# Performance work log

Measured on AMD Instinct MI355X. Metric: run time of the kernel, lower is better.

Reference implementation:

```python
import jax, jax.numpy as jnp
import numpy as np

B, L, A = 256, 512, 40          # proteins, residues per protein, atoms per drug
FD, FT, LD = 78, 54, 128        # drug feat, protein feat, latent dim
P = L + 1                       # residues + 1 appended drug super-node


def setup_inputs() -> dict:
    key = jax.random.key(0)
    ks = iter(jax.random.split(key, 48))
    Nd = B * A
    # drug graphs: chain bonds, both directions
    i = np.arange(A - 1)
    s = np.concatenate([i, i + 1]); d = np.concatenate([i + 1, i])
    off = (np.arange(B) * A)[:, None]
    drug_ei = jnp.asarray(np.stack([(s[None] + off).ravel(), (d[None] + off).ravel()]), jnp.int32)
    drug_batch = jnp.asarray(np.repeat(np.arange(B), A), jnp.int32)
    # protein graphs: residue chain + drug super-node (local idx L) connected to all residues in order
    r = np.arange(L - 1)
    ps = np.concatenate([r, r + 1, np.full(L, L), np.arange(L)])
    pd = np.concatenate([r + 1, r, np.arange(L), np.full(L, L)])
    poff = (np.arange(B) * P)[:, None]
    prot_ei = jnp.asarray(np.stack([(ps[None] + poff).ravel(), (pd[None] + poff).ravel()]), jnp.int32)
    prot_batch = jnp.asarray(np.repeat(np.arange(B), P), jnp.int32)
    E2 = B * (2 * (L - 1) + 2 * L)

    def lin(fi, fo):
        return jax.random.normal(next(ks), (fi, fo), jnp.float32) / np.float32(np.sqrt(fi))

    def vec(fo):
        return jnp.zeros((fo,), jnp.float32)

    return dict(
        drug_x=jax.random.normal(next(ks), (Nd, FD), jnp.float32),
        drug_ei=drug_ei, drug_batch=drug_batch,
        prot_x=jax.random.normal(next(ks), (B * P, FT), jnp.float32),
        prot_ei=prot_ei, prot_batch=prot_batch,
        prot_ea=jax.random.uniform(next(ks), (E2,), jnp.float32),
        W_c1d=lin(FD, FD), b_c1d=vec(FD),
        W_c2d=lin(FD, 2 * FD), b_c2d=vec(2 * FD),
        W_rd_g=lin(2 * FD, 2 * FD), b_rd_g=vec(2 * FD), W_rd_l=lin(2 * FD, 2 * FD),
        W_fg1d=lin(2 * FD, 1024), b_fg1d=vec(1024),
        W_fg2d=lin(1024, FT), b_fg2d=vec(FT),
        W_fg3d=lin(FT, 2 * LD), b_fg3d=vec(2 * LD),
        W_att1=lin(FT, FT), b_att1=vec(FT),
        W_att2=lin(FT, 1), b_att2=vec(1),
        W_c1t=lin(FT, LD), b_c1t=vec(LD),
        W_c2t=lin(LD, 2 * LD), b_c2t=vec(2 * LD),
        W_rt_g=lin(2 * LD, 2 * LD), b_rt_g=vec(2 * LD), W_rt_l=lin(2 * LD, 2 * LD),
        W_fg1t=lin(2 * LD, 1024), b_fg1t=vec(1024),
        W_fg2t=lin(1024, 2 * LD), b_fg2t=vec(2 * LD),
        W_fc1=lin(4 * LD, 1024), b_fc1=vec(1024),
        W_fc2=lin(1024, 512), b_fc2=vec(512),
        W_out=lin(512, 1), b_out=vec(1),
    )


def _gcn(x, W, b, src, dst, ew, n):
    # PyG GCNConv: symmetric norm with self-loops (fill value 1), optional edge weights
    h = x @ W
    deg = jax.ops.segment_sum(ew, dst, num_segments=n) + 1.0
    dinv = jax.lax.rsqrt(deg)
    norm = dinv[src] * ew * dinv[dst]
    agg = jax.ops.segment_sum(h[src] * norm[:, None], dst, num_segments=n)
    return agg + h * (dinv * dinv)[:, None] + b


def _rblock(x, Wg, bg, Wl, src, dst, ew, n):
    h = jax.nn.relu(_gcn(x, Wg, bg, src, dst, ew, n))
    return jax.nn.relu(h @ Wl + x)


def reference(drug_x, drug_ei, drug_batch, prot_x, prot_ei, prot_batch, prot_ea,
              W_c1d, b_c1d, W_c2d, b_c2d, W_rd_g, b_rd_g, W_rd_l,
              W_fg1d, b_fg1d, W_fg2d, b_fg2d, W_fg3d, b_fg3d,
              W_att1, b_att1, W_att2, b_att2,
              W_c1t, b_c1t, W_c2t, b_c2t, W_rt_g, b_rt_g, W_rt_l,
              W_fg1t, b_fg1t, W_fg2t, b_fg2t,
              W_fc1, b_fc1, W_fc2, b_fc2, W_out, b_out):
    relu = jax.nn.relu
    Nd, N2 = drug_x.shape[0], prot_x.shape[0]
    sd, dd = drug_ei[0], drug_ei[1]
    ewd = jnp.ones(sd.shape[0], drug_x.dtype)
    x = relu(_gcn(drug_x, W_c1d, b_c1d, sd, dd, ewd, Nd))
    x = relu(_gcn(x, W_c2d, b_c2d, sd, dd, ewd, Nd))
    for _ in range(4):  # shared-weight residual block applied num_rblock times
        x = _rblock(x, W_rd_g, b_rd_g, W_rd_l, sd, dd, ewd, Nd)
    xg = jax.ops.segment_max(x, drug_batch, num_segments=B)  # global max pool
    x = relu(xg @ W_fg1d + b_fg1d)
    x = x @ W_fg2d + b_fg2d                                   # [B, FT]
    x_chg = relu(x @ W_fg3d + b_fg3d)                          # [B, 2*LD]
    # vectorized per-protein attention (replaces the python loop over prot_lens)
    res = prot_x.reshape(B, P, FT)[:, :L]                      # residues only
    att = jnp.tanh(res @ W_att1 + b_att1) @ W_att2 + b_att2    # [B, L, 1]
    att = jax.nn.softmax(att[..., 0], axis=1)                  # [B, L]
    att_node = jnp.concatenate([att, jnp.zeros((B, 1), att.dtype)], 1).reshape(-1)
    drug_idx = (jnp.arange(B) + 1) * P - 1
    is_drug = jnp.zeros((N2,), bool).at[drug_idx].set(True)
    st, dt = prot_ei[0], prot_ei[1]
    # edges touching a drug super-node get that residue's attention weight
    ea = jnp.where(is_drug[st], att_node[dt], jnp.where(is_drug[dt], att_node[st], prot_ea))
    x2 = prot_x.at[drug_idx].set(x)                            # inject drug embeddings
    x2 = relu(_gcn(x2, W_c1t, b_c1t, st, dt, ea, N2))
    x2 = relu(_gcn(x2, W_c2t, b_c2t, st, dt, ea, N2))
    ew1 = jnp.ones(st.shape[0], x2.dtype)
    for _ in range(4):
        x2 = _rblock(x2, W_rt_g, b_rt_g, W_rt_l, st, dt, ew1, N2)
    x2r = x2.reshape(B, P, 2 * LD)
    x2g = x2r[:, :L].max(axis=1)                               # gmp over residues (drug node masked out)
    drug_after = x2r[:, L]
    x2v = relu(x2g @ W_fg1t + b_fg1t) @ W_fg2t + b_fg2t
    xm = jnp.maximum(drug_after, x_chg)                        # max_pool1d(kernel=2) over the pair
    xc = jnp.concatenate([xm, x2v], 1)
    xc = relu(xc @ W_fc1 + b_fc1)
    xc = relu(xc @ W_fc2 + b_fc2)
    return xc @ W_out + b_out
```

## Files before the change

### kernel.cpp

```cpp
#include <hip/hip_runtime.h>
#include <cstdio>

#define B_   256
#define L_   512
#define A_   40
#define FD_  78
#define FT_  54
#define LD_  128
#define P_   513
#define ND_  (B_*A_)
#define N2_  (B_*P_)
#define EB_  2046

typedef __attribute__((ext_vector_type(8))) short short8;
typedef __attribute__((ext_vector_type(4))) float floatx4;
typedef unsigned short u16;

__device__ __forceinline__ short f2bf(float f) {
    union { float f; unsigned u; } v; v.f = f;
    unsigned u = v.u;
    u += 0x7fff + ((u >> 16) & 1);
    return (short)(u >> 16);
}
__device__ __forceinline__ float bf2f(u16 s) {
    union { unsigned u; float f; } v; v.u = ((unsigned)s) << 16; return v.f;
}

#define TBK 32
#define LDK 40
#define UBS 264

__global__ __launch_bounds__(256) void gemm_mfma_k(
    const float* __restrict__ A, const short* __restrict__ WT,
    float* __restrict__ C, int M, int N, int K, int Kp)
{
    __shared__ short As[128 * LDK];
    __shared__ short Bs[128 * LDK];
    const int bm = blockIdx.y * 128;
    const int bn = blockIdx.x * 128;
    const int tid  = threadIdx.x;
    const int wave = tid >> 6, lane = tid & 63;
    const int wm = (wave >> 1) * 64, wn = (wave & 1) * 64;
    const int lrow = lane & 15, quad = lane >> 4;

    floatx4 acc[4][4] = {};

    for (int k0 = 0; k0 < Kp; k0 += TBK) {
#pragma unroll
        for (int it = 0; it < 2; ++it) {
            int g   = it * 256 + tid;
            int row = g >> 2, kg = g & 3;
            int kb  = k0 + kg * 8;
            const float* arow = A + (size_t)(bm + row) * K + kb;
            short8 av;
#pragma unroll
            for (int j = 0; j < 8; ++j) av[j] = (kb + j < K) ? f2bf(arow[j]) : (short)0;
            *(short8*)&As[row * LDK + kg * 8] = av;
            *(short8*)&Bs[row * LDK + kg * 8] = *(const short8*)(WT + (size_t)(bn + row) * Kp + kb);
        }
        __syncthreads();
        short8 af[4], bfv[4];
#pragma unroll
        for (int i = 0; i < 4; ++i)
            af[i] = *(short8*)&As[(wm + i * 16 + lrow) * LDK + quad * 8];
#pragma unroll
        for (int j = 0; j < 4; ++j)
            bfv[j] = *(short8*)&Bs[(wn + j * 16 + lrow) * LDK + quad * 8];
#pragma unroll
        for (int i = 0; i < 4; ++i)
#pragma unroll
            for (int j = 0; j < 4; ++j)
                acc[i][j] = __builtin_amdgcn_mfma_f32_16x16x32_bf16(af[i], bfv[j], acc[i][j], 0, 0, 0);
        __syncthreads();
    }
#pragma unroll
    for (int i = 0; i < 4; ++i) {
        int grow0 = bm + wm + i * 16 + quad * 4;
#pragma unroll
        for (int j = 0; j < 4; ++j) {
            int col = bn + wn + j * 16 + lrow;
            size_t base = (size_t)grow0 * N + col;
#pragma unroll
            for (int r = 0; r < 4; ++r)
                C[base + (size_t)r * N] = acc[i][j][r];
        }
    }
}

__global__ __launch_bounds__(256) void gemm_bb_k(
    const u16* __restrict__ A, int lda, const short* __restrict__ WT, int Kp,
    const u16* __restrict__ resid, u16* __restrict__ C, int N, int act)
{
    __shared__ short As[128 * LDK];
    __shared__ short Bs[128 * LDK];
    const int bm = blockIdx.y * 128;
    const int bn = blockIdx.x * 128;
    const int tid  = threadIdx.x;
    const int wave = tid >> 6, lane = tid & 63;
    const int wm = (wave >> 1) * 64, wn = (wave & 1) * 64;
    const int lrow = lane & 15, quad = lane >> 4;

    floatx4 acc[4][4] = {};

    for (int k0 = 0; k0 < Kp; k0 += TBK) {
#pragma unroll
        for (int it = 0; it < 2; ++it) {
            int g   = it * 256 + tid;
            int row = g >> 2, kg = g & 3;
            int kb  = k0 + kg * 8;
            *(short8*)&As[row * LDK + kg * 8] = *(const short8*)(A + (size_t)(bm + row) * lda + kb);
            *(short8*)&Bs[row * LDK + kg * 8] = *(const short8*)(WT + (size_t)(bn + row) * Kp + kb);
        }
        __syncthreads();
        short8 af[4], bfv[4];
#pragma unroll
        for (int i = 0; i < 4; ++i)
            af[i] = *(short8*)&As[(wm + i * 16 + lrow) * LDK + quad * 8];
#pragma unroll
        for (int j = 0; j < 4; ++j)
            bfv[j] = *(short8*)&Bs[(wn + j * 16 + lrow) * LDK + quad * 8];
#pragma unroll
        for (int i = 0; i < 4; ++i)
#pragma unroll
            for (int j = 0; j < 4; ++j)
                acc[i][j] = __builtin_amdgcn_mfma_f32_16x16x32_bf16(af[i], bfv[j], acc[i][j], 0, 0, 0);
        __syncthreads();
    }
#pragma unroll
    for (int i = 0; i < 4; ++i) {
        int grow0 = bm + wm + i * 16 + quad * 4;
#pragma unroll
        for (int j = 0; j < 4; ++j) {
            int col = bn + wn + j * 16 + lrow;
            size_t base = (size_t)grow0 * N + col;
#pragma unroll
            for (int r = 0; r < 4; ++r) {
                float v = acc[i][j][r];
                size_t idx = base + (size_t)r * N;
                if (resid) v += bf2f(resid[idx]);
                if (act)   v = fmaxf(v, 0.f);
                C[idx] = (u16)f2bf(v);
            }
        }
    }
}

template<int KT>
__global__ __launch_bounds__(256, 3) void gemm_n256pw_k(
    const u16* __restrict__ A, const short* __restrict__ WT,
    const u16* __restrict__ resid, u16* __restrict__ C, int act,
    const float* __restrict__ cInF, float* __restrict__ Wacc)
{
    constexpr int K = KT * TBK;
    __shared__ short As[64 * LDK];
    __shared__ short Bs[256 * LDK];
    const int bm = blockIdx.x * 64;
    const int tid  = threadIdx.x;
    const int wave = tid >> 6, lane = tid & 63;
    const int wn = wave * 64;
    const int lrow = lane & 15, quad = lane >> 4;
    const int srow = tid >> 2, skg = tid & 3;

    floatx4 acc[4][4] = {};

    short8 aR[KT];
#pragma unroll
    for (int kt = 0; kt < KT; ++kt)
        aR[kt] = *(const short8*)(A + (size_t)(bm + srow) * K + kt * TBK + skg * 8);
    short8 bReg[4];
#pragma unroll
    for (int it = 0; it < 4; ++it)
        bReg[it] = *(const short8*)(WT + (size_t)(it * 64 + srow) * K + skg * 8);

#pragma unroll
    for (int kt = 0; kt < KT; ++kt) {
        *(short8*)&As[srow * LDK + skg * 8] = aR[kt];
#pragma unroll
        for (int it = 0; it < 4; ++it)
            *(short8*)&Bs[(it * 64 + srow) * LDK + skg * 8] = bReg[it];
        __syncthreads();
        if (kt + 1 < KT) {
            int kn = (kt + 1) * TBK;
#pragma unroll
            for (int it = 0; it < 4; ++it)
                bReg[it] = *(const short8*)(WT + (size_t)(it * 64 + srow) * K + kn + skg * 8);
        }
        short8 af[4], bfv[4];
#pragma unroll
        for (int i = 0; i < 4; ++i)
            af[i] = *(short8*)&As[(i * 16 + lrow) * LDK + quad * 8];
#pragma unroll
        for (int j = 0; j < 4; ++j)
            bfv[j] = *(short8*)&Bs[(wn + j * 16 + lrow) * LDK + quad * 8];
#pragma unroll
        for (int i = 0; i < 4; ++i)
#pragma unroll
            for (int j = 0; j < 4; ++j)
                acc[i][j] = __builtin_amdgcn_mfma_f32_16x16x32_bf16(af[i], bfv[j], acc[i][j], 0, 0, 0);
        __syncthreads();
    }
#pragma unroll
    for (int i = 0; i < 4; ++i) {
        int grow0 = bm + i * 16 + quad * 4;
#pragma unroll
        for (int j = 0; j < 4; ++j) {
            int col = wn + j * 16 + lrow;
            size_t base = (size_t)grow0 * 256 + col;
#pragma unroll
            for (int r = 0; r < 4; ++r) {
                float v = acc[i][j][r];
                size_t idx = base + (size_t)r * 256;
                if (resid) v += bf2f(resid[idx]);
                if (act)   v = fmaxf(v, 0.f);
                C[idx] = (u16)f2bf(v);
            }
        }
    }
    if (cInF) {
        const int b0 = bm / P_;
        const int b1 = (bm + 63) / P_;
        float s0[4] = {0.f, 0.f, 0.f, 0.f};
        float s1[4] = {0.f, 0.f, 0.f, 0.f};
#pragma unroll
        for (int i = 0; i < 4; ++i) {
#pragma unroll
            for (int r = 0; r < 4; ++r) {
                int grow = bm + i * 16 + quad * 4 + r;
                float ci = cInF[grow];
                bool hi = (grow / P_) != b0;
#pragma unroll
                for (int j = 0; j < 4; ++j) {
                    float v = ci * acc[i][j][r];
                    if (hi) s1[j] += v; else s0[j] += v;
                }
            }
        }
#pragma unroll
        for (int j = 0; j < 4; ++j) {
            s0[j] += __shfl_xor(s0[j], 16);
            s0[j] += __shfl_xor(s0[j], 32);
            s1[j] += __shfl_xor(s1[j], 16);
            s1[j] += __shfl_xor(s1[j], 32);
        }
        if (quad == 0) {
#pragma unroll
            for (int j = 0; j < 4; ++j) {
                int col = wn + j * 16 + lrow;
                atomicAdd(&Wacc[(size_t)b0 * 256 + col], s0[j]);
                if (b1 != b0) atomicAdd(&Wacc[(size_t)b1 * 256 + col], s1[j]);
            }
        }
    }
}

static inline void gemm_n256(const u16* A, int K, const short* WT,
                             const u16* resid, u16* C, int act,
                             const float* cInF, float* Wacc, hipStream_t s)
{
    dim3 g(N2_ / 64), b(256);
    if (K == 128)
        hipLaunchKernelGGL((gemm_n256pw_k<4>), g, b, 0, s, A, WT, resid, C, act, cInF, Wacc);
    else
        hipLaunchKernelGGL((gemm_n256pw_k<8>), g, b, 0, s, A, WT, resid, C, act, cInF, Wacc);
}

template<int KT>
__global__ __launch_bounds__(256, 2) void fused_res_k(
    const u16* __restrict__ X, const short* __restrict__ WTg,
    const short* __restrict__ WTl, const u16* __restrict__ Udrug,
    const float* __restrict__ cPc, const float* __restrict__ cNc,
    const float* __restrict__ cDc, const float* __restrict__ cSc,
    const float* __restrict__ cInF, const float* __restrict__ bias_g,
    float* __restrict__ Wacc, u16* __restrict__ Xn)
{
    constexpr int K = KT * TBK;
    __shared__ short Ub[80 * UBS];
    __shared__ short As[80 * LDK];
    const int bm    = blockIdx.x * 64;
    const int gbase = bm - 8;
    const int tid   = threadIdx.x;
    const int wave  = tid >> 6, lane = tid & 63;
    const int wn    = wave * 64;
    const int lrow  = lane & 15, quad = lane >> 4;
    const int srow  = tid >> 2, skg = tid & 3;

    int g1 = gbase + srow;
    g1 = g1 < 0 ? 0 : g1;
    const u16* ap1 = X + (size_t)g1 * K + skg * 8;
    int g2 = gbase + 64 + srow;
    g2 = g2 >= N2_ ? N2_ - 1 : g2;
    const u16* ap2 = X + (size_t)g2 * K + skg * 8;
    const bool w0 = (wave == 0);

    const short* bgp0 = WTg + (size_t)(wn +  0 + lrow) * K + quad * 8;
    const short* bgp1 = WTg + (size_t)(wn + 16 + lrow) * K + quad * 8;
    const short* bgp2 = WTg + (size_t)(wn + 32 + lrow) * K + quad * 8;
    const short* bgp3 = WTg + (size_t)(wn + 48 + lrow) * K + quad * 8;

    floatx4 acc[5][4] = {};
    short8 aP1[2], aP2[2], bP[2][4];
    aP1[0] = *(const short8*)ap1;
    if (w0) aP2[0] = *(const short8*)ap2;
    bP[0][0] = *(const short8*)bgp0;
    bP[0][1] = *(const short8*)bgp1;
    bP[0][2] = *(const short8*)bgp2;
    bP[0][3] = *(const short8*)bgp3;

#pragma unroll
    for (int kt = 0; kt < KT; ++kt) {
        const int cur = kt & 1, nxt = cur ^ 1;
        *(short8*)&As[srow * LDK + skg * 8] = aP1[cur];
        if (w0) *(short8*)&As[(64 + srow) * LDK + skg * 8] = aP2[cur];
        __syncthreads();
        if (kt + 1 < KT) {
            const int kn = (kt + 1) * TBK;
            aP1[nxt] = *(const short8*)(ap1 + kn);
            if (w0) aP2[nxt] = *(const short8*)(ap2 + kn);
            bP[nxt][0] = *(const short8*)(bgp0 + kn);
            bP[nxt][1] = *(const short8*)(bgp1 + kn);
            bP[nxt][2] = *(const short8*)(bgp2 + kn);
            bP[nxt][3] = *(const short8*)(bgp3 + kn);
        }
        short8 af[5];
#pragma unroll
        for (int i = 0; i < 5; ++i)
            af[i] = *(short8*)&As[(i * 16 + lrow) * LDK + quad * 8];
#pragma unroll
        for (int i = 0; i < 5; ++i)
#pragma unroll
            for (int j = 0; j < 4; ++j)
                acc[i][j] = __builtin_amdgcn_mfma_f32_16x16x32_bf16(af[i], bP[cur][j], acc[i][j], 0, 0, 0);
        __syncthreads();
    }

    {
        const int b0 = bm / P_;
        const int b1 = (bm + 63) / P_;
        float s0[4] = {0.f, 0.f, 0.f, 0.f};
        float s1[4] = {0.f, 0.f, 0.f, 0.f};
#pragma unroll
        for (int i = 0; i < 5; ++i) {
#pragma unroll
            for (int r = 0; r < 4; ++r) {
                int wr = i * 16 + quad * 4 + r;
                if (wr >= 8 && wr < 72) {
                    int grow = gbase + wr;
                    float ci = cInF[grow];
                    bool hi = (grow / P_) != b0;
#pragma unroll
                    for (int j = 0; j < 4; ++j) {
                        float v = ci * acc[i][j][r];
                        if (hi) s1[j] += v; else s0[j] += v;
                    }
                }
            }
        }
#pragma unroll
        for (int j = 0; j < 4; ++j) {
            s0[j] += __shfl_xor(s0[j], 16);
            s0[j] += __shfl_xor(s0[j], 32);
            s1[j] += __shfl_xor(s1[j], 16);
            s1[j] += __shfl_xor(s1[j], 32);
        }
        if (quad == 0) {
#pragma unroll
            for (int j = 0; j < 4; ++j) {
                int col = wn + j * 16 + lrow;
                atomicAdd(&Wacc[(size_t)b0 * 256 + col], s0[j]);
                if (b1 != b0) atomicAdd(&Wacc[(size_t)b1 * 256 + col], s1[j]);
            }
        }
    }

#pragma unroll
    for (int i = 0; i < 5; ++i)
#pragma unroll
        for (int r = 0; r < 4; ++r) {
            int wr = i * 16 + quad * 4 + r;
#pragma unroll
            for (int j = 0; j < 4; ++j)
                Ub[wr * UBS + wn + j * 16 + lrow] = f2bf(acc[i][j][r]);
        }
    __syncthreads();

    const int r    = bm + srow;
    const int bl   = r / P_;
    const int irow = r - bl * P_;
    const bool isD = (irow == L_);
    const float cs = isD ? 0.f : cSc[r];
    const float cp = isD ? 0.f : cPc[r];
    const float cn = isD ? 0.f : cNc[r];
    const float cd = isD ? 0.f : cDc[r];
    const u16* udp = Udrug + (size_t)bl * 256;

    const short* blp0 = WTl + (size_t)(wn +  0 + lrow) * K + quad * 8;
    const short* blp1 = WTl + (size_t)(wn + 16 + lrow) * K + quad * 8;
    const short* blp2 = WTl + (size_t)(wn + 32 + lrow) * K + quad * 8;
    const short* blp3 = WTl + (size_t)(wn + 48 + lrow) * K + quad * 8;

    floatx4 acc2[4][4] = {};
    short8 bl2[2][4];
    bl2[0][0] = *(const short8*)blp0;
    bl2[0][1] = *(const short8*)blp1;
    bl2[0][2] = *(const short8*)blp2;
    bl2[0][3] = *(const short8*)blp3;

#pragma unroll
    for (int kt = 0; kt < KT; ++kt) {
        const int cur = kt & 1, nxt = cur ^ 1;
        const int c0 = kt * TBK + skg * 8;
        short8 uS = *(short8*)&Ub[(8 + srow) * UBS + c0];
        short8 uM = *(short8*)&Ub[(7 + srow) * UBS + c0];
        short8 uP = *(short8*)&Ub[(9 + srow) * UBS + c0];
        short8 ud = *(const short8*)(udp + c0);
        float4 bi0 = *(const float4*)(bias_g + c0);
        float4 bi1 = *(const float4*)(bias_g + c0 + 4);
        float bv[8] = {bi0.x, bi0.y, bi0.z, bi0.w, bi1.x, bi1.y, bi1.z, bi1.w};
        short8 av;
#pragma unroll
        for (int e = 0; e < 8; ++e) {
            float v = cs * bf2f((u16)uS[e]) + cp * bf2f((u16)uM[e])
                    + cn * bf2f((u16)uP[e]) + cd * bf2f((u16)ud[e]) + bv[e];
            av[e] = f2bf(fmaxf(v, 0.f));
        }
        *(short8*)&As[srow * LDK + skg * 8] = av;
        __syncthreads();
        if (kt + 1 < KT) {
            const int kn = (kt + 1) * TBK;
            bl2[nxt][0] = *(const short8*)(blp0 + kn);
            bl2[nxt][1] = *(const short8*)(blp1 + kn);
            bl2[nxt][2] = *(const short8*)(blp2 + kn);
            bl2[nxt][3] = *(const short8*)(blp3 + kn);
        }
        short8 af2[4];
#pragma unroll
        for (int i = 0; i < 4; ++i)
            af2[i] = *(short8*)&As[(i * 16 + lrow) * LDK + quad * 8];
#pragma unroll
        for (int i = 0; i < 4; ++i)
#pragma unroll
            for (int j = 0; j < 4; ++j)
                acc2[i][j] = __builtin_amdgcn_mfma_f32_16x16x32_bf16(af2[i], bl2[cur][j], acc2[i][j], 0, 0, 0);
        __syncthreads();
    }

#pragma unroll
    for (int i = 0; i < 4; ++i) {
        int grow0 = bm + i * 16 + quad * 4;
#pragma unroll
        for (int j = 0; j < 4; ++j) {
            int col = wn + j * 16 + lrow;
            size_t base = (size_t)grow0 * 256 + col;
#pragma unroll
            for (int r2 = 0; r2 < 4; ++r2) {
                float v = acc2[i][j][r2];
                size_t idx = base + (size_t)r2 * 256;
                v += bf2f(X[idx]);
                v = fmaxf(v, 0.f);
                Xn[idx] = (u16)f2bf(v);
            }
        }
    }
}

__global__ __launch_bounds__(256) void udrug_k(
    const u16* __restrict__ Xold, const short* __restrict__ WTg,
    u16* __restrict__ Udrug)
{
    __shared__ float xr[256];
    int b = blockIdx.x, t = threadIdx.x;
    size_t rD = (size_t)b * P_ + L_;
    xr[t] = bf2f(Xold[rD * 256 + t]);
    __syncthreads();
    const short* wrow = WTg + (size_t)t * 256;
    float v = 0.f;
    for (int k = 0; k < 256; k += 8) {
        short8 w = *(const short8*)(wrow + k);
#pragma unroll
        for (int e = 0; e < 8; ++e) v += xr[k + e] * bf2f((u16)w[e]);
    }
    Udrug[(size_t)b * 256 + t] = (u16)f2bf(v);
}

__global__ __launch_bounds__(256) void drug_row_k(
    const float* __restrict__ Wacc, const u16* __restrict__ Udrug,
    const float* __restrict__ cSc, const float* __restrict__ bias_g,
    const short* __restrict__ WTl, const u16* __restrict__ Xold,
    u16* __restrict__ Xn)
{
    __shared__ float a2[256];
    int b = blockIdx.x, t = threadIdx.x;
    size_t rD = (size_t)b * P_ + L_;
    float u = bf2f(Udrug[(size_t)b * 256 + t]);
    float av = fmaxf(Wacc[(size_t)b * 256 + t] + cSc[rD] * u + bias_g[t], 0.f);
    a2[t] = bf2f((u16)f2bf(av));
    __syncthreads();
    const short* wrow = WTl + (size_t)t * 256;
    float v = 0.f;
    for (int k = 0; k < 256; k += 8) {
        short8 w = *(const short8*)(wrow + k);
#pragma unroll
        for (int e = 0; e < 8; ++e) v += a2[k + e] * bf2f((u16)w[e]);
    }
    v += bf2f(Xold[rD * 256 + t]);
    Xn[rD * 256 + t] = (u16)f2bf(fmaxf(v, 0.f));
}

__global__ void wt_cvt_k(const float* __restrict__ W, short* __restrict__ WT,
                         int K, int Nreal, int Kp, int Ntot)
{
    int idx = blockIdx.x * 256 + threadIdx.x;
    if (idx >= Ntot * Kp) return;
    int n = idx / Kp, k = idx - n * Kp;
    WT[idx] = (k < K && n < Nreal) ? f2bf(W[(size_t)k * Nreal + n]) : (short)0;
}

#define BM 64
#define BN 64
#define BKK 16
__global__ __launch_bounds__(256) void gemm_k(
    const float* __restrict__ Amat, const float* __restrict__ Wmat,
    const float* __restrict__ bias, const float* __restrict__ resid,
    float* __restrict__ Cmat, int M, int N, int K, int act)
{
    __shared__ float As[BKK][BM + 4];
    __shared__ float Ws[BKK][BN];
    const int bm = blockIdx.y * BM;
    const int bn = blockIdx.x * BN;
    const int tx = threadIdx.x, ty = threadIdx.y;
    const int tid = ty * 16 + tx;
    float acc[4][4] = {};

    for (int k0 = 0; k0 < K; k0 += BKK) {
#pragma unroll
        for (int j = 0; j < 4; ++j) {
            int l = tid + 256 * j;
            int m = l >> 4, kk = l & 15;
            int gm = bm + m, gk = k0 + kk;
            As[kk][m] = (gm < M && gk < K) ? Amat[(size_t)gm * K + gk] : 0.f;
        }
#pragma unroll
        for (int j = 0; j < 4; ++j) {
            int l = tid + 256 * j;
            int kk = l >> 6, n = l & 63;
            int gk = k0 + kk, gn = bn + n;
            Ws[kk][n] = (gk < K && gn < N) ? Wmat[(size_t)gk * N + gn] : 0.f;
        }
        __syncthreads();
#pragma unroll
        for (int k = 0; k < BKK; ++k) {
            float4 a4 = *(const float4*)&As[k][ty * 4];
            float4 w4 = *(const float4*)&Ws[k][tx * 4];
            float av[4] = {a4.x, a4.y, a4.z, a4.w};
            float wv[4] = {w4.x, w4.y, w4.z, w4.w};
#pragma unroll
            for (int i = 0; i < 4; ++i)
#pragma unroll
                for (int j = 0; j < 4; ++j)
                    acc[i][j] = fmaf(av[i], wv[j], acc[i][j]);
        }
        __syncthreads();
    }
#pragma unroll
    for (int i = 0; i < 4; ++i) {
        int gm = bm + ty * 4 + i;
        if (gm >= M) continue;
#pragma unroll
        for (int j = 0; j < 4; ++j) {
            int gn = bn + tx * 4 + j;
            if (gn >= N) continue;
            float v = acc[i][j];
            if (bias)  v += bias[gn];
            if (resid) v += resid[(size_t)gm * N + gn];
            if (act)   v = fmaxf(v, 0.f);
            Cmat[(size_t)gm * N + gn] = v;
        }
    }
}

static inline void gemm(const float* A, const float* W, const float* bias,
                        const float* resid, float* C, int M, int N, int K, int act,
                        hipStream_t s)
{
    dim3 g((N + BN - 1) / BN, (M + BM - 1) / BM), b(16, 16);
    hipLaunchKernelGGL(gemm_k, g, b, 0, s, A, W, bias, resid, C, M, N, K, act);
}

__global__ __launch_bounds__(256) void gemm_skA_k(
    const float* __restrict__ Amat, const float* __restrict__ Wmat,
    float* __restrict__ part, int M, int N, int K, int Kc)
{
    __shared__ float As[BKK][BM + 4];
    __shared__ float Ws[BKK][BN];
    const int bm = blockIdx.y * BM;
    const int bn = blockIdx.x * BN;
    const int sk = blockIdx.z;
    const int kb0  = sk * Kc;
    const int kend = min(K, kb0 + Kc);
    const int tx = threadIdx.x, ty = threadIdx.y;
    const int tid = ty * 16 + tx;
    float acc[4][4] = {};

    for (int k0 = kb0; k0 < kend; k0 += BKK) {
#pragma unroll
        for (int j = 0; j < 4; ++j) {
            int l = tid + 256 * j;
            int m = l >> 4, kk = l & 15;
            int gm = bm + m, gk = k0 + kk;
            As[kk][m] = (gm < M && gk < kend) ? Amat[(size_t)gm * K + gk] : 0.f;
        }
#pragma unroll
        for (int j = 0; j < 4; ++j) {
            int l = tid + 256 * j;
            int kk = l >> 6, n = l & 63;
            int gk = k0 + kk, gn = bn + n;
            Ws[kk][n] = (gk < kend && gn < N) ? Wmat[(size_t)gk * N + gn] : 0.f;
        }
        __syncthreads();
#pragma unroll
        for (int k = 0; k < BKK; ++k) {
            float4 a4 = *(const float4*)&As[k][ty * 4];
            float4 w4 = *(const float4*)&Ws[k][tx * 4];
            float av[4] = {a4.x, a4.y, a4.z, a4.w};
            float wv[4] = {w4.x, w4.y, w4.z, w4.w};
#pragma unroll
            for (int i = 0; i < 4; ++i)
#pragma unroll
                for (int j = 0; j < 4; ++j)
                    acc[i][j] = fmaf(av[i], wv[j], acc[i][j]);
        }
        __syncthreads();
    }
#pragma unroll
    for (int i = 0; i < 4; ++i) {
        int gm = bm + ty * 4 + i;
        if (gm >= M) continue;
#pragma unroll
        for (int j = 0; j < 4; ++j) {
            int gn = bn + tx * 4 + j;
            if (gn >= N) continue;
            part[((size_t)sk * M + gm) * N + gn] = acc[i][j];
        }
    }
}

__global__ void gemm_skB_k(const float* __restrict__ part, const float* __restrict__ bias,
                           float* __restrict__ C, int M, int N, int SK, int act)
{
    int idx = blockIdx.x * 256 + threadIdx.x;
    if (idx >= M * N) return;
    int n = idx % N;
    float v = bias ? bias[n] : 0.f;
    for (int s = 0; s < SK; ++s) v += part[(size_t)s * M * N + idx];
    if (act) v = fmaxf(v, 0.f);
    C[idx] = v;
}

static inline void gemm_sk(const float* A, const float* W, const float* bias,
                           float* C, float* skbuf, int M, int N, int K, int SK, int act,
                           hipStream_t s)
{
    int Kc = (K + SK - 1) / SK;
    dim3 g((N + 63) / 64, (M + 63) / 64, SK), b(16, 16);
    hipLaunchKernelGGL(gemm_skA_k, g, b, 0, s, A, W, skbuf, M, N, K, Kc);
    hipLaunchKernelGGL(gemm_skB_k, dim3((M * N + 255) / 256), dim3(256), 0, s,
                       skbuf, bias, C, M, N, SK, act);
}

__global__ void drug_agg_k(const float* __restrict__ h, const float* __restrict__ bias,
                           float* __restrict__ out, int F)
{
    int r = blockIdx.x;
    int a = r % A_;
    int t = threadIdx.x;
    if (t >= F) return;
    const float DI2 = 0.70710678118654752f;
    const float DI3 = 0.57735026918962576f;
    float da = (a == 0 || a == A_ - 1) ? DI2 : DI3;
    const float* hs = h + (size_t)r * F;
    float v = da * da * hs[t] + bias[t];
    if (a > 0) {
        float dp = (a - 1 == 0) ? DI2 : DI3;
        v += dp * da * hs[t - F];
    }
    if (a < A_ - 1) {
        float dn = (a + 1 == A_ - 1) ? DI2 : DI3;
        v += dn * da * hs[t + F];
    }
    out[(size_t)r * F + t] = fmaxf(v, 0.f);
}

__global__ void drug_max_k(const float* __restrict__ x, float* __restrict__ xg)
{
    int b = blockIdx.x, t = threadIdx.x;
    if (t >= 2 * FD_) return;
    const float* xb = x + (size_t)b * A_ * (2 * FD_);
    float m = -INFINITY;
    for (int a = 0; a < A_; ++a) m = fmaxf(m, xb[a * (2 * FD_) + t]);
    xg[b * (2 * FD_) + t] = m;
}

__global__ __launch_bounds__(256) void att_dot_k(
    const float* __restrict__ Hs, const float* __restrict__ b1,
    const float* __restrict__ W2, const float* __restrict__ b2,
    float* __restrict__ scores)
{
    int w = threadIdx.x >> 6, lane = threadIdx.x & 63;
    float b1v = (lane < FT_) ? b1[lane] : 0.f;
    float w2v = (lane < FT_) ? W2[lane] : 0.f;
    float b2v = b2[0];
    int base = blockIdx.x * 64 + w * 16;
    for (int rr = 0; rr < 16; ++rr) {
        int r = base + rr;
        float v = 0.f;
        if (lane < FT_) v = tanhf(Hs[(size_t)r * 128 + lane] + b1v) * w2v;
#pragma unroll
        for (int o = 32; o; o >>= 1) v += __shfl_down(v, o);
        if (lane == 0) {
            int bl = r / P_, i = r - bl * P_;
            if (i < L_) scores[bl * L_ + i] = v + b2v;
        }
    }
}

__global__ __launch_bounds__(512) void softmax_k(
    const float* __restrict__ scores, float* __restrict__ att, float* __restrict__ attsum)
{
    int b = blockIdx.x, t = threadIdx.x;
    __shared__ float sm[8];
    __shared__ float bcast;
    float v = scores[b * L_ + t];
    float m = v;
#pragma unroll
    for (int o = 32; o; o >>= 1) m = fmaxf(m, __shfl_down(m, o));
    if ((t & 63) == 0) sm[t >> 6] = m;
    __syncthreads();
    if (t == 0) { float mm = sm[0]; for (int i = 1; i < 8; ++i) mm = fmaxf(mm, sm[i]); bcast = mm; }
    __syncthreads();
    float mx = bcast;
    float e = expf(v - mx);
    float s = e;
#pragma unroll
    for (int o = 32; o; o >>= 1) s += __shfl_down(s, o);
    __syncthreads();
    if ((t & 63) == 0) sm[t >> 6] = s;
    __syncthreads();
    if (t == 0) { float ss = 0; for (int i = 0; i < 8; ++i) ss += sm[i]; bcast = ss; }
    __syncthreads();
    float a = e / bcast;
    att[b * L_ + t] = a;
    float s2 = a;
#pragma unroll
    for (int o = 32; o; o >>= 1) s2 += __shfl_down(s2, o);
    __syncthreads();
    if ((t & 63) == 0) sm[t >> 6] = s2;
    __syncthreads();
    if (t == 0) { float ss = 0; for (int i = 0; i < 8; ++i) ss += sm[i]; attsum[b] = ss; }
}

__global__ void coef_deg_k(const float* __restrict__ prot_ea, const float* __restrict__ att,
                           const float* __restrict__ attsum, float* __restrict__ dinv, int use_ea)
{
    int r = blockIdx.x * 256 + threadIdx.x;
    if (r >= N2_) return;
    int b = r / P_, i = r - b * P_;
    float deg;
    if (i == L_) {
        deg = 1.f + (use_ea ? attsum[b] : (float)L_);
    } else {
        float wP = (i >= 1)      ? (use_ea ? prot_ea[b * EB_ + (i - 1)]   : 1.f) : 0.f;
        float wN = (i <= L_ - 2) ? (use_ea ? prot_ea[b * EB_ + 511 + i]   : 1.f) : 0.f;
        float wD = use_ea ? att[b * L_ + i] : 1.f;
        deg = 1.f + wP + wN + wD;
    }
    dinv[r] = rsqrtf(deg);
}

__global__ void coef_k(const float* __restrict__ dinv, const float* __restrict__ prot_ea,
                       const float* __restrict__ att, float* __restrict__ cP, float* __restrict__ cN,
                       float* __restrict__ cD, float* __restrict__ cS, float* __restrict__ cIn,
                       float* __restrict__ cInF, int use_ea)
{
    int r = blockIdx.x * 256 + threadIdx.x;
    if (r >= N2_) return;
    int b = r / P_, i = r - b * P_;
    float di = dinv[r];
    cS[r] = di * di;
    if (i == L_) { cP[r] = 0.f; cN[r] = 0.f; cD[r] = 0.f; cInF[r] = 0.f; return; }
    float wP = (i >= 1)      ? (use_ea ? prot_ea[b * EB_ + (i - 1)] : 1.f) : 0.f;
    float wN = (i <= L_ - 2) ? (use_ea ? prot_ea[b * EB_ + 511 + i] : 1.f) : 0.f;
    float wD = use_ea ? att[b * L_ + i] : 1.f;
    float dD = dinv[b * P_ + L_];
    cP[r] = (i >= 1)      ? dinv[r - 1] * wP * di : 0.f;
    cN[r] = (i <= L_ - 2) ? dinv[r + 1] * wN * di : 0.f;
    cD[r] = dD * wD * di;
    float ci = di * wD * dD;
    cIn[b * L_ + i] = ci;
    cInF[r] = ci;
}

template<int F>
__global__ __launch_bounds__(256) void prot_agg_res_k(
    const u16* __restrict__ h, const float* __restrict__ cP,
    const float* __restrict__ cN, const float* __restrict__ cD,
    const float* __restrict__ cS, const float* __restrict__ cIn,
    const float* __restrict__ bias, u16* __restrict__ outp,
    float* __restrict__ Wacc)
{
    constexpr int G = F / 8;
    constexpr int RPB = 256 / G;
    __shared__ float pacc[RPB * F];
    int t = threadIdx.x;
    int rl = t / G, g = t - rl * G;
    int base = blockIdx.x * RPB;
    int r = base + rl;
    int bl = r / P_, i = r - bl * P_;
    int f0 = g * 8;
    const u16* hs = h + (size_t)r * F + f0;
    if (i == L_) {
#pragma unroll
        for (int e = 0; e < 8; ++e) pacc[rl * F + f0 + e] = 0.f;
    } else {
        const u16* hd = h + ((size_t)bl * P_ + L_) * F + f0;
        float cs = cS[r], cd = cD[r], cp = cP[r], cn = cN[r];
        float ci = cIn[bl * L_ + i];
        short8 vs = *(const short8*)hs;
        short8 vd = *(const short8*)hd;
        short8 vp = *(const short8*)(hs - (i > 0 ? F : 0));
        short8 vn = *(const short8*)(hs + F);
        short8 ov;
#pragma unroll
        for (int e = 0; e < 8; ++e) {
            float hv = bf2f((u16)vs[e]);
            pacc[rl * F + f0 + e] = ci * hv;
            float v = cs * hv + cd * bf2f((u16)vd[e]) + bias[f0 + e];
            v += cp * bf2f((u16)vp[e]);
            v += cn * bf2f((u16)vn[e]);
            ov[e] = f2bf(fmaxf(v, 0.f));
        }
        *(short8*)(outp + (size_t)r * F + f0) = ov;
    }
    __syncthreads();
    int f = t;
    if (f < F) {
        int b0   = base / P_;
        int bend = (base + RPB - 1) / P_;
        float s0 = 0.f, s1 = 0.f;
#pragma unroll
        for (int rr = 0; rr < RPB; ++rr) {
            float v = pacc[rr * F + f];
            if ((base + rr) / P_ == b0) s0 += v; else s1 += v;
        }
        atomicAdd(&Wacc[(size_t)b0 * F + f], s0);
        if (bend != b0) atomicAdd(&Wacc[(size_t)bend * F + f], s1);
    }
}

__global__ void drug_fin_k(const float* __restrict__ Wacc, const u16* __restrict__ h,
                           const float* __restrict__ cS, const float* __restrict__ bias,
                           u16* __restrict__ outp, int F)
{
    int bl = blockIdx.x, t = threadIdx.x;
    if (t >= F) return;
    size_t rD = (size_t)bl * P_ + L_;
    float v = Wacc[(size_t)bl * F + t] + cS[rD] * bf2f(h[rD * F + t]) + bias[t];
    outp[rD * F + t] = (u16)f2bf(fmaxf(v, 0.f));
}

__global__ void xin_k(const float* __restrict__ prot_x, const float* __restrict__ t2d,
                      u16* __restrict__ Xin)
{
    int idx = blockIdx.x * 256 + threadIdx.x;
    if (idx >= N2_ * 64) return;
    int r = idx >> 6, t = idx & 63;
    int bl = r / P_, i = r - bl * P_;
    float v = 0.f;
    if (t < FT_) v = (i == L_) ? t2d[bl * FT_ + t] : prot_x[(size_t)r * FT_ + t];
    Xin[idx] = (u16)f2bf(v);
}

__global__ __launch_bounds__(256) void x2g_bf2_k(const u16* __restrict__ X,
                                                 float* __restrict__ x2g, float* __restrict__ da)
{
    __shared__ float red[2048];
    int t = threadIdx.x;
    int rl = t >> 5, g = t & 31;
    int bl = blockIdx.x, f0 = g * 8;
    const u16* xb = X + (size_t)bl * P_ * 256;
    float m[8];
#pragma unroll
    for (int e = 0; e < 8; ++e) m[e] = -INFINITY;
    for (int j = rl; j < L_; j += 8) {
        short8 v = *(const short8*)(xb + (size_t)j * 256 + f0);
#pragma unroll
        for (int e = 0; e < 8; ++e) m[e] = fmaxf(m[e], bf2f((u16)v[e]));
    }
#pragma unroll
    for (int e = 0; e < 8; ++e) red[rl * 256 + f0 + e] = m[e];
    __syncthreads();
    if (rl == 0) {
        short8 vd = *(const short8*)(xb + (size_t)L_ * 256 + f0);
#pragma unroll
        for (int e = 0; e < 8; ++e) {
            float v = red[f0 + e];
            for (int rr = 1; rr < 8; ++rr) v = fmaxf(v, red[rr * 256 + f0 + e]);
            x2g[bl * 256 + f0 + e] = v;
            da[bl * 256 + f0 + e] = bf2f((u16)vd[e]);
        }
    }
}

__global__ void build_xc_k(const float* __restrict__ da, const float* __restrict__ x_chg,
                           const float* __restrict__ x2v, float* __restrict__ xc)
{
    int idx = blockIdx.x * 256 + threadIdx.x;
    if (idx >= B_ * 512) return;
    int b = idx >> 9, c = idx & 511;
    float v = (c < 256) ? fmaxf(da[b * 256 + c], x_chg[b * 256 + c])
                        : x2v[b * 256 + (c - 256)];
    xc[idx] = v;
}

__global__ __launch_bounds__(64) void out_k(const float* __restrict__ f2,
                                            const float* __restrict__ W,
                                            const float* __restrict__ bias,
                                            float* __restrict__ out)
{
    int row = blockIdx.x, t = threadIdx.x;
    float v = 0.f;
    for (int k = t; k < 512; k += 64) v = fmaf(f2[(size_t)row * 512 + k], W[k], v);
#pragma unroll
    for (int o = 32; o; o >>= 1) v += __shfl_down(v, o);
    if (t == 0) out[row] = v + bias[0];
}

extern "C" void kernel_launch(void* const* d_in, const int* in_sizes, int n_in,
                              void* d_out, int out_size, void* d_ws, size_t ws_size,
                              hipStream_t stream)
{
    const float* drug_x  = (const float*)d_in[0];
    const float* prot_x  = (const float*)d_in[3];
    const float* prot_ea = (const float*)d_in[6];
    const float* W_c1d = (const float*)d_in[7];   const float* b_c1d = (const float*)d_in[8];
    const float* W_c2d = (const float*)d_in[9];   const float* b_c2d = (const float*)d_in[10];
    const float* W_rd_g = (const float*)d_in[11]; const float* b_rd_g = (const float*)d_in[12];
    const float* W_rd_l = (const float*)d_in[13];
    const float* W_fg1d = (const float*)d_in[14]; const float* b_fg1d = (const float*)d_in[15];
    const float* W_fg2d = (const float*)d_in[16]; const float* b_fg2d = (const float*)d_in[17];
    const float* W_fg3d = (const float*)d_in[18]; const float* b_fg3d = (const float*)d_in[19];
    const float* W_att1 = (const float*)d_in[20]; const float* b_att1 = (const float*)d_in[21];
    const float* W_att2 = (const float*)d_in[22]; const float* b_att2 = (const float*)d_in[23];
    const float* W_c1t = (const float*)d_in[24];  const float* b_c1t = (const float*)d_in[25];
    const float* W_c2t = (const float*)d_in[26];  const float* b_c2t = (const float*)d_in[27];
    const float* W_rt_g = (const float*)d_in[28]; const float* b_rt_g = (const float*)d_in[29];
    const float* W_rt_l = (const float*)d_in[30];
    const float* W_fg1t = (const float*)d_in[31]; const float* b_fg1t = (const float*)d_in[32];
    const float* W_fg2t = (const float*)d_in[33]; const float* b_fg2t = (const float*)d_in[34];
    const float* W_fc1 = (const float*)d_in[35];  const float* b_fc1 = (const float*)d_in[36];
    const float* W_fc2 = (const float*)d_in[37];  const float* b_fc2 = (const float*)d_in[38];
    const float* W_out = (const float*)d_in[39];  const float* b_out = (const float*)d_in[40];
    float* out = (float*)d_out;

    float* ws = (float*)d_ws;
    size_t off = 0;
    auto alloc = [&](size_t n) {
        n = (n + 3) & ~(size_t)3;
        float* p = ws + off; off += n; return p;
    };

    u16* U = (u16*)alloc((size_t)N2_ * 128);
    u16* V = (u16*)alloc((size_t)N2_ * 128);
    u16* X = (u16*)alloc((size_t)N2_ * 128);
    u16* Xin = (u16*)alloc((size_t)N2_ * 32);
    float* Hs = (float*)U;
    float* Wacc = alloc(B_ * 256);
    u16* Udrug = (u16*)alloc(B_ * 128);
    float* dA = alloc((size_t)ND_ * 156);
    float* dB = alloc((size_t)ND_ * 156);
    float* dC = alloc((size_t)ND_ * 156);
    float* xg    = alloc(B_ * 156);
    float* t1d   = alloc(B_ * 1024);
    float* t2d   = alloc(B_ * FT_);
    float* x_chg = alloc(B_ * 256);
    float* scores = alloc(B_ * 512);
    float* att    = alloc(B_ * 512);
    float* attsum = alloc(B_);
    float* dinvE = alloc(N2_);
    float* cPE = alloc(N2_); float* cNE = alloc(N2_); float* cDE = alloc(N2_); float* cSE = alloc(N2_);
    float* cInE = alloc(B_ * 512);
    float* cInFE = alloc(N2_);
    float* dinvO = alloc(N2_);
    float* cPO = alloc(N2_); float* cNO = alloc(N2_); float* cDO = alloc(N2_); float* cSO = alloc(N2_);
    float* cInO = alloc(B_ * 512);
    float* cInFO = alloc(N2_);
    float* x2g = alloc(B_ * 256);
    float* dafter = alloc(B_ * 256);
    float* t1t = alloc(B_ * 1024);
    float* x2v = alloc(B_ * 256);
    float* xc  = alloc(B_ * 512);
    float* f1  = alloc(B_ * 1024);
    float* f2  = alloc(B_ * 512);
    float* skbuf = alloc((size_t)2 * 1024 * 1024);
    short* WT_c1t = (short*)alloc(128 * 64 / 2);
    short* WT_c2t = (short*)alloc(256 * 128 / 2);
    short* WT_rtg = (short*)alloc(256 * 256 / 2);
    short* WT_rtl = (short*)alloc(256 * 256 / 2);
    short* WT_att = (short*)alloc(128 * 64 / 2);

    if (off * sizeof(float) > ws_size) {
        fprintf(stderr, "kernel_launch: workspace too small: need %zu, have %zu\n",
                off * sizeof(float), ws_size);
        return;
    }

    hipLaunchKernelGGL(wt_cvt_k, dim3((128 * 64 + 255) / 256), dim3(256), 0, stream,  W_c1t, WT_c1t, FT_, 128, 64, 128);
    hipLaunchKernelGGL(wt_cvt_k, dim3((256 * 128 + 255) / 256), dim3(256), 0, stream, W_c2t, WT_c2t, 128, 256, 128, 256);
    hipLaunchKernelGGL(wt_cvt_k, dim3((256 * 256 + 255) / 256), dim3(256), 0, stream, W_rt_g, WT_rtg, 256, 256, 256, 256);
    hipLaunchKernelGGL(wt_cvt_k, dim3((256 * 256 + 255) / 256), dim3(256), 0, stream, W_rt_l, WT_rtl, 256, 256, 256, 256);
    hipLaunchKernelGGL(wt_cvt_k, dim3((128 * 64 + 255) / 256), dim3(256), 0, stream,  W_att1, WT_att, FT_, FT_, 64, 128);

    gemm(drug_x, W_c1d, nullptr, nullptr, dB, ND_, FD_, FD_, 0, stream);
    hipLaunchKernelGGL(drug_agg_k, dim3(ND_), dim3(128), 0, stream, dB, b_c1d, dA, FD_);
    gemm(dA, W_c2d, nullptr, nullptr, dB, ND_, 2 * FD_, FD_, 0, stream);
    hipLaunchKernelGGL(drug_agg_k, dim3(ND_), dim3(192), 0, stream, dB, b_c2d, dA, 2 * FD_);
    for (int it = 0; it < 4; ++it) {
        gemm(dA, W_rd_g, nullptr, nullptr, dB, ND_, 2 * FD_, 2 * FD_, 0, stream);
        hipLaunchKernelGGL(drug_agg_k, dim3(ND_), dim3(192), 0, stream, dB, b_rd_g, dC, 2 * FD_);
        gemm(dC, W_rd_l, nullptr, dA, dB, ND_, 2 * FD_, 2 * FD_, 1, stream);
        float* tmp = dA; dA = dB; dB = tmp;
    }
    hipLaunchKernelGGL(drug_max_k, dim3(B_), dim3(192), 0, stream, dA, xg);
    gemm_sk(xg,  W_fg1d, b_fg1d, t1d,   skbuf, B_, 1024, 156, 4, 1, stream);
    gemm_sk(t1d, W_fg2d, b_fg2d, t2d,   skbuf, B_, FT_, 1024, 16, 0, stream);
    gemm_sk(t2d, W_fg3d, b_fg3d, x_chg, skbuf, B_, 2 * LD_, FT_, 2, 1, stream);

    {
        dim3 g(1, N2_ / 128), b(256);
        hipLaunchKernelGGL(gemm_mfma_k, g, b, 0, stream, prot_x, WT_att, Hs, N2_, 128, FT_, 64);
    }
    hipLaunchKernelGGL(att_dot_k, dim3(N2_ / 64), dim3(256), 0, stream, Hs, b_att1, W_att2, b_att2, scores);
    hipLaunchKernelGGL(softmax_k, dim3(B_), dim3(512), 0, stream, scores, att, attsum);

    hipLaunchKernelGGL(coef_deg_k, dim3((N2_ + 255) / 256), dim3(256), 0, stream, prot_ea, att, attsum, dinvE, 1);
    hipLaunchKernelGGL(coef_k, dim3((N2_ + 255) / 256), dim3(256), 0, stream, dinvE, prot_ea, att, cPE, cNE, cDE, cSE, cInE, cInFE, 1);
    hipLaunchKernelGGL(coef_deg_k, dim3((N2_ + 255) / 256), dim3(256), 0, stream, prot_ea, att, attsum, dinvO, 0);
    hipLaunchKernelGGL(coef_k, dim3((N2_ + 255) / 256), dim3(256), 0, stream, dinvO, prot_ea, att, cPO, cNO, cDO, cSO, cInO, cInFO, 0);

    hipLaunchKernelGGL(xin_k, dim3((N2_ * 64 + 255) / 256), dim3(256), 0, stream, prot_x, t2d, Xin);

    {
        dim3 g(1, N2_ / 128), b(256);
        hipLaunchKernelGGL(gemm_bb_k, g, b, 0, stream, Xin, 64, WT_c1t, 64,
                           (const u16*)nullptr, U, 128, 0);
    }
    hipMemsetAsync(Wacc, 0, B_ * 128 * sizeof(float), stream);
    hipLaunchKernelGGL((prot_agg_res_k<128>), dim3(N2_ / 16), dim3(256), 0, stream,
                       U, cPE, cNE, cDE, cSE, cInE, b_c1t, V, Wacc);
    hipLaunchKernelGGL(drug_fin_k, dim3(B_), dim3(128), 0, stream, Wacc, U, cSE, b_c1t, V, 128);
    gemm_n256(V, 128, WT_c2t, (const u16*)nullptr, U, 0, nullptr, nullptr, stream);
    hipMemsetAsync(Wacc, 0, B_ * 256 * sizeof(float), stream);
    hipLaunchKernelGGL((prot_agg_res_k<256>), dim3(N2_ / 8), dim3(256), 0, stream,
                       U, cPE, cNE, cDE, cSE, cInE, b_c2t, X, Wacc);
    hipLaunchKernelGGL(drug_fin_k, dim3(B_), dim3(256), 0, stream, Wacc, U, cSE, b_c2t, X, 256);

    u16* Xc = X;
    u16* Xo = U;
    for (int it = 0; it < 4; ++it) {
        hipMemsetAsync(Wacc, 0, B_ * 256 * sizeof(float), stream);
        hipLaunchKernelGGL(udrug_k, dim3(B_), dim3(256), 0, stream, Xc, WT_rtg, Udrug);
        hipLaunchKernelGGL((fused_res_k<8>), dim3(N2_ / 64), dim3(256), 0, stream,
                           Xc, WT_rtg, WT_rtl, Udrug,
                           cPO, cNO, cDO, cSO, cInFO, b_rt_g, Wacc, Xo);
        hipLaunchKernelGGL(drug_row_k, dim3(B_), dim3(256), 0, stream,
                           Wacc, Udrug, cSO, b_rt_g, WT_rtl, Xc, Xo);
        u16* t = Xc; Xc = Xo; Xo = t;
    }

    hipLaunchKernelGGL(x2g_bf2_k, dim3(B_), dim3(256), 0, stream, Xc, x2g, dafter);

    gemm_sk(x2g, W_fg1t, b_fg1t, t1t, skbuf, B_, 1024, 256, 8, 1, stream);
    gemm_sk(t1t, W_fg2t, b_fg2t, x2v, skbuf, B_, 256, 1024, 16, 0, stream);
    hipLaunchKernelGGL(build_xc_k, dim3(B_ * 512 / 256), dim3(256), 0, stream, dafter, x_chg, x2v, xc);
    gemm_sk(xc, W_fc1, b_fc1, f1, skbuf, B_, 1024, 512, 8, 1, stream);
    gemm_sk(f1, W_fc2, b_fc2, f2, skbuf, B_, 512, 1024, 16, 1, stream);
    hipLaunchKernelGGL(out_k, dim3(B_), dim3(64), 0, stream, f2, W_out, b_out, out);
}
```

Baseline: 1.348 ms.

## Preload A tiles into registers, XOR-swizzle Ub, fuse udrug and memset into drug_row

In fused_res_k, all K-slices of the A rows are now loaded into registers up front instead of double-buffered per step. The padded Ub staging buffer is replaced by an unpadded XOR-swizzled layout to cut LDS bank conflicts and shared memory use. drug_row_k now zeroes Wacc and computes the next iteration's Udrug itself, so the per-iteration memset and udrug_k launches are removed. This adds register pressure, which may reduce occupancy, and adds serial work to the small drug_row kernel.

```diff
diff --git a/kernel.cpp b/kernel.cpp
--- a/kernel.cpp
+++ b/kernel.cpp
@@ -28,7 +28,6 @@
 
 #define TBK 32
 #define LDK 40
-#define UBS 264
 
 __global__ __launch_bounds__(256) void gemm_mfma_k(
     const float* __restrict__ A, const short* __restrict__ WT,
@@ -273,8 +272,9 @@
     const float* __restrict__ cInF, const float* __restrict__ bias_g,
     float* __restrict__ Wacc, u16* __restrict__ Xn)
 {
-    constexpr int K = KT * TBK;
-    __shared__ short Ub[80 * UBS];
+    constexpr int K   = KT * TBK;
+    constexpr int UBW = 256;
+    __shared__ short Ub[80 * UBW];
     __shared__ short As[80 * LDK];
     const int bm    = blockIdx.x * 64;
     const int gbase = bm - 8;
@@ -292,15 +292,24 @@
     const u16* ap2 = X + (size_t)g2 * K + skg * 8;
     const bool w0 = (wave == 0);
 
+    short8 aR1[KT];
+#pragma unroll
+    for (int kt = 0; kt < KT; ++kt)
+        aR1[kt] = *(const short8*)(ap1 + kt * TBK);
+    short8 aR2[KT];
+    if (w0) {
+#pragma unroll
+        for (int kt = 0; kt < KT; ++kt)
+            aR2[kt] = *(const short8*)(ap2 + kt * TBK);
+    }
+
     const short* bgp0 = WTg + (size_t)(wn +  0 + lrow) * K + quad * 8;
     const short* bgp1 = WTg + (size_t)(wn + 16 + lrow) * K + quad * 8;
     const short* bgp2 = WTg + (size_t)(wn + 32 + lrow) * K + quad * 8;
     const short* bgp3 = WTg + (size_t)(wn + 48 + lrow) * K + quad * 8;
 
     floatx4 acc[5][4] = {};
-    short8 aP1[2], aP2[2], bP[2][4];
-    aP1[0] = *(const short8*)ap1;
-    if (w0) aP2[0] = *(const short8*)ap2;
+    short8 bP[2][4];
     bP[0][0] = *(const short8*)bgp0;
     bP[0][1] = *(const short8*)bgp1;
     bP[0][2] = *(const short8*)bgp2;
@@ -309,13 +318,11 @@
 #pragma unroll
     for (int kt = 0; kt < KT; ++kt) {
         const int cur = kt & 1, nxt = cur ^ 1;
-        *(short8*)&As[srow * LDK + skg * 8] = aP1[cur];
-        if (w0) *(short8*)&As[(64 + srow) * LDK + skg * 8] = aP2[cur];
+        *(short8*)&As[srow * LDK + skg * 8] = aR1[kt];
+        if (w0) *(short8*)&As[(64 + srow) * LDK + skg * 8] = aR2[kt];
         __syncthreads();
         if (kt + 1 < KT) {
             const int kn = (kt + 1) * TBK;
-            aP1[nxt] = *(const short8*)(ap1 + kn);
-            if (w0) aP2[nxt] = *(const short8*)(ap2 + kn);
             bP[nxt][0] = *(const short8*)(bgp0 + kn);
             bP[nxt][1] = *(const short8*)(bgp1 + kn);
             bP[nxt][2] = *(const short8*)(bgp2 + kn);
@@ -377,9 +384,10 @@
 #pragma unroll
         for (int r = 0; r < 4; ++r) {
             int wr = i * 16 + quad * 4 + r;
+            int x  = (wr & 7) << 3;
 #pragma unroll
             for (int j = 0; j < 4; ++j)
-                Ub[wr * UBS + wn + j * 16 + lrow] = f2bf(acc[i][j][r]);
+                Ub[wr * UBW + ((wn + j * 16 + lrow) ^ x)] = f2bf(acc[i][j][r]);
         }
     __syncthreads();
 
@@ -405,13 +413,16 @@
     bl2[0][2] = *(const short8*)blp2;
     bl2[0][3] = *(const short8*)blp3;
 
+    const int rM = 7 + srow, rS = 8 + srow, rP = 9 + srow;
+    const int xM = (rM & 7) << 3, xS = (rS & 7) << 3, xP = (rP & 7) << 3;
+
 #pragma unroll
     for (int kt = 0; kt < KT; ++kt) {
         const int cur = kt & 1, nxt = cur ^ 1;
         const int c0 = kt * TBK + skg * 8;
-        short8 uS = *(short8*)&Ub[(8 + srow) * UBS + c0];
-        short8 uM = *(short8*)&Ub[(7 + srow) * UBS + c0];
-        short8 uP = *(short8*)&Ub[(9 + srow) * UBS + c0];
+        short8 uS = *(short8*)&Ub[rS * UBW + (c0 ^ xS)];
+        short8 uM = *(short8*)&Ub[rM * UBW + (c0 ^ xM)];
+        short8 uP = *(short8*)&Ub[rP * UBW + (c0 ^ xP)];
         short8 ud = *(const short8*)(udp + c0);
         float4 bi0 = *(const float4*)(bias_g + c0);
         float4 bi1 = *(const float4*)(bias_g + c0 + 4);
@@ -483,27 +494,42 @@
 }
 
 __global__ __launch_bounds__(256) void drug_row_k(
-    const float* __restrict__ Wacc, const u16* __restrict__ Udrug,
+    float* __restrict__ Wacc, u16* __restrict__ Udrug,
     const float* __restrict__ cSc, const float* __restrict__ bias_g,
-    const short* __restrict__ WTl, const u16* __restrict__ Xold,
-    u16* __restrict__ Xn)
+    const short* __restrict__ WTl, const short* __restrict__ WTg,
+    const u16* __restrict__ Xold, u16* __restrict__ Xn, int last)
 {
     __shared__ float a2[256];
+    __shared__ float xn[256];
     int b = blockIdx.x, t = threadIdx.x;
     size_t rD = (size_t)b * P_ + L_;
     float u = bf2f(Udrug[(size_t)b * 256 + t]);
     float av = fmaxf(Wacc[(size_t)b * 256 + t] + cSc[rD] * u + bias_g[t], 0.f);
+    Wacc[(size_t)b * 256 + t] = 0.f;
     a2[t] = bf2f((u16)f2bf(av));
     __syncthreads();
-    const short* wrow = WTl + (size_t)t * 256;
+    const short* wl = WTl + (size_t)t * 256;
     float v = 0.f;
     for (int k = 0; k < 256; k += 8) {
-        short8 w = *(const short8*)(wrow + k);
+        short8 w = *(const short8*)(wl + k);
 #pragma unroll
         for (int e = 0; e < 8; ++e) v += a2[k + e] * bf2f((u16)w[e]);
     }
     v += bf2f(Xold[rD * 256 + t]);
-    Xn[rD * 256 + t] = (u16)f2bf(fmaxf(v, 0.f));
+    u16 xb = (u16)f2bf(fmaxf(v, 0.f));
+    Xn[rD * 256 + t] = xb;
+    if (!last) {
+        xn[t] = bf2f(xb);
+        __syncthreads();
+        const short* wg = WTg + (size_t)t * 256;
+        float v2 = 0.f;
+        for (int k = 0; k < 256; k += 8) {
+            short8 w = *(const short8*)(wg + k);
+#pragma unroll
+            for (int e = 0; e < 8; ++e) v2 += xn[k + e] * bf2f((u16)w[e]);
+        }
+        Udrug[(size_t)b * 256 + t] = (u16)f2bf(v2);
+    }
 }
 
 __global__ void wt_cvt_k(const float* __restrict__ W, short* __restrict__ WT,
@@ -1063,16 +1089,16 @@
                        U, cPE, cNE, cDE, cSE, cInE, b_c2t, X, Wacc);
     hipLaunchKernelGGL(drug_fin_k, dim3(B_), dim3(256), 0, stream, Wacc, U, cSE, b_c2t, X, 256);
 
+    hipMemsetAsync(Wacc, 0, B_ * 256 * sizeof(float), stream);
     u16* Xc = X;
     u16* Xo = U;
+    hipLaunchKernelGGL(udrug_k, dim3(B_), dim3(256), 0, stream, Xc, WT_rtg, Udrug);
     for (int it = 0; it < 4; ++it) {
-        hipMemsetAsync(Wacc, 0, B_ * 256 * sizeof(float), stream);
-        hipLaunchKernelGGL(udrug_k, dim3(B_), dim3(256), 0, stream, Xc, WT_rtg, Udrug);
         hipLaunchKernelGGL((fused_res_k<8>), dim3(N2_ / 64), dim3(256), 0, stream,
                            Xc, WT_rtg, WT_rtl, Udrug,
                            cPO, cNO, cDO, cSO, cInFO, b_rt_g, Wacc, Xo);
         hipLaunchKernelGGL(drug_row_k, dim3(B_), dim3(256), 0, stream,
-                           Wacc, Udrug, cSO, b_rt_g, WT_rtl, Xc, Xo);
+                           Wacc, Udrug, cSO, b_rt_g, WT_rtl, WT_rtg, Xc, Xo, it == 3);
         u16* t = Xc; Xc = Xo; Xo = t;
     }
 
```

New measurement: 1.366 ms. Within noise of the previous version (+1.3%).
